# Performance work log

Hardware: AMD Instinct MI355X
Metric: run time of the kernel (lower is better)

The kernel has to match this reference:

```python
import jax, jax.numpy as jnp
from jax import lax
import numpy as np

# ---- init hyperparameters (from init_kwargs) ----
STRIDE = 1
DP_CHANNELS = 1
ATOM_R = 8
ATOM_C = 8
NUMB_ATOM = 128
T_SC = 3
K = 256
BATCH = 32
IMG = 64


def setup_inputs() -> dict:
    key = jax.random.key(0)
    k1, k2 = jax.random.split(key)
    Y = jax.random.normal(k1, (BATCH, DP_CHANNELS, IMG, IMG), dtype=jnp.float32)
    # ConvTranspose2d weight layout: (numb_atom, dp_channels, atom_c, atom_r)
    W = jax.random.normal(k2, (NUMB_ATOM, DP_CHANNELS, ATOM_C, ATOM_R), dtype=jnp.float32)
    # normalise_weights(): each (i, j) filter divided by its L2 norm
    W = W / jnp.sqrt(jnp.sum(W ** 2, axis=(2, 3), keepdims=True))
    return {"Y": Y, "W_D": W}


def _conv_D(X, W):
    # PyTorch ConvTranspose2d (stride=1, no padding): full convolution with
    # spatially-flipped kernel; W is (in=numb_atom, out=dp_channels, kh, kw).
    kh, kw = W.shape[2], W.shape[3]
    return lax.conv_general_dilated(
        X, jnp.flip(W, (2, 3)), (1, 1),
        [(kh - 1, kh - 1), (kw - 1, kw - 1)],
        dimension_numbers=('NCHW', 'IOHW', 'NCHW'))


def _conv_Dt(R, Wt):
    # PyTorch Conv2d (VALID, stride=1): Wt is (out=numb_atom, in=dp, kh, kw)
    return lax.conv_general_dilated(
        R, Wt, (1, 1), 'VALID', dimension_numbers=('NCHW', 'OIHW', 'NCHW'))


def _hard_threshold_k(X, k):
    # keep the k largest-|.| entries per sample (over flattened C,H,W)
    B = X.shape[0]
    flat = X.reshape(B, -1)
    _, idx = lax.top_k(jnp.abs(flat), k)                      # [B, k]
    vals = jnp.take_along_axis(flat, idx, axis=1)             # [B, k]
    out = jnp.zeros_like(flat).at[jnp.arange(B)[:, None], idx].set(vals)
    return out.reshape(X.shape)


def _linesearch(Y, X, W, Wt, k):
    R = Y - _conv_D(X, W)
    g = _conv_Dt(R, Wt)
    l2_start = jnp.sum(R ** 2)

    def attempt(alpha):
        Xu = _hard_threshold_k(X + alpha * g, k)
        err = jnp.sum((Y - _conv_D(Xu, W)) ** 2)
        return Xu, err

    Xu0, err0 = attempt(jnp.float32(1.0))

    def cond(s):
        _, _, err, count = s
        return (err >= l2_start) & (count <= 15)

    def body(s):
        alpha, _, _, count = s
        alpha = alpha * jnp.float32(0.5)
        Xu, err = attempt(alpha)
        return (alpha, Xu, err, count + 1)

    alpha, Xu, err, _ = lax.while_loop(
        cond, body, (jnp.float32(1.0), Xu0, err0, jnp.int32(0)))
    return Xu, err, alpha


def reference(Y, W_D):
    # D_trans.weight = D.weight.permute(0,1,3,2) -> (numb_atom, dp, atom_r, atom_c)
    Wt = jnp.swapaxes(W_D, 2, 3)
    kh, kw = Wt.shape[2], Wt.shape[3]
    B, _, H, W_sp = Y.shape
    X = jnp.zeros((B, W_D.shape[0], H - kh + 1, W_sp - kw + 1), dtype=Y.dtype)
    for _ in range(T_SC):
        X, _, _ = _linesearch(Y, X, W_D, Wt, K)
    return X
```

## Files before the change

kernel.cpp:

```cpp
#include <hip/hip_runtime.h>
#include <stdint.h>

#define NB   32
#define NCH  128
#define IMG  64
#define IMG2 4096
#define OH   57
#define OHW  3249
#define CHW  415872
#define KTOP 256
#define NATT 17
#define NS   32
#define SCAP 512
#define CAP2 8192
#define NCAP 2048
#define NBUCK 8192
#define HSHIFT 18
#define TGT  512
#define RSTRIDE 72
#define NZB  257

__global__ void k_init(int* support_cnt) {
    if (threadIdx.x < NB) support_cnt[threadIdx.x] = 0;
}

__global__ __launch_bounds__(256) void k_resid(
    const float* __restrict__ Y, const float* __restrict__ W,
    const int* __restrict__ support_cnt, const uint32_t* __restrict__ support_idx,
    const float* __restrict__ support_val, float* __restrict__ Rg, double* __restrict__ l2part,
    uint32_t* __restrict__ hist, int* __restrict__ cand_cnt)
{
    int bx = blockIdx.x, tid = threadIdx.x;
    if (bx >= NB) {
        int zb = bx - NB;
        if (zb < 256) {
            ((uint4*)hist)[zb * 256 + tid] = make_uint4(0u, 0u, 0u, 0u);
        } else {
            ((uint4*)cand_cnt)[tid] = make_uint4(0u, 0u, 0u, 0u);
        }
        return;
    }
    int b = bx;
    __shared__ float Rs[IMG2];
    const float4* Y4 = (const float4*)(Y + b * IMG2);
    float4* R4 = (float4*)Rs;
    for (int i = tid; i < IMG2 / 4; i += 256) R4[i] = Y4[i];
    __syncthreads();
    int n = support_cnt[b];
    for (int task = tid; task < n * 64; task += 256) {
        int i = task >> 6, tap = task & 63, p = tap >> 3, q = tap & 7;
        uint32_t idx = support_idx[b * KTOP + i];
        float val = support_val[b * KTOP + i];
        int c = idx / OHW, rem = idx % OHW, s = rem / OH, t = rem % OH;
        float w = W[c * 64 + p * 8 + q];
        atomicAdd(&Rs[(s + p) * IMG + (t + q)], -val * w);
    }
    __syncthreads();
    double acc = 0.0;
    for (int i = tid; i < IMG2; i += 256) {
        float v = Rs[i];
        Rg[b * IMG2 + i] = v;
        acc += (double)v * (double)v;
    }
    __shared__ double red[256];
    red[tid] = acc; __syncthreads();
    for (int s2 = 128; s2 > 0; s2 >>= 1) { if (tid < s2) red[tid] += red[tid + s2]; __syncthreads(); }
    if (tid == 0) l2part[b] = red[0];
}

__global__ __launch_bounds__(256) void k_conv(
    const float* __restrict__ Rg, const float* __restrict__ W,
    float* __restrict__ g_out, uint32_t* __restrict__ hist)
{
    int b = blockIdx.x, cg0 = blockIdx.y, tid = threadIdx.x;
    __shared__ float Rs[71 * 72];
    __shared__ uint32_t hl[NBUCK];
    for (int i = tid; i < 71 * 72; i += 256) Rs[i] = 0.f;
    for (int i = tid; i < NBUCK; i += 256) hl[i] = 0u;
    __syncthreads();
    const float4* R4 = (const float4*)(Rg + b * IMG2);
    for (int i = tid; i < 1024; i += 256) {
        int row = i >> 4, col4 = (i & 15) * 4;
        *(float4*)&Rs[row * 72 + col4] = R4[i];
    }
    __syncthreads();
    int csub = tid >> 7;
    int tile = tid & 127;
    bool active = tile < 120;
    int tr = active ? tile / 15 : 0;
    int tc = active ? tile % 15 : 0;
    int s0 = tr * 8, t0 = tc * 4;

    for (int sub = 0; sub < 4; ++sub) {
        int c = cg0 * 8 + sub * 2 + csub;
        int c_s = __builtin_amdgcn_readfirstlane(c);
        const float* Wc = W + c_s * 64;

        float acc[8][4];
#pragma unroll
        for (int r = 0; r < 8; ++r)
#pragma unroll
            for (int cc = 0; cc < 4; ++cc) acc[r][cc] = 0.f;

#pragma unroll
        for (int rho = 0; rho < 15; ++rho) {
            float rb[12];
            const float* rp = &Rs[(s0 + rho) * 72 + t0];
            *(float4*)&rb[0] = *(const float4*)rp;
            *(float4*)&rb[4] = *(const float4*)(rp + 4);
            *(float4*)&rb[8] = *(const float4*)(rp + 8);
#pragma unroll
            for (int r = 0; r < 8; ++r) {
                const int p = rho - r;
                if (p >= 0 && p < 8) {
#pragma unroll
                    for (int q = 0; q < 8; ++q) {
                        float wv = Wc[q * 8 + p];
#pragma unroll
                        for (int cc = 0; cc < 4; ++cc)
                            acc[r][cc] = fmaf(rb[cc + q], wv, acc[r][cc]);
                    }
                }
            }
        }
        if (active) {
            float* go = g_out + (size_t)(b * NCH + c) * OHW;
#pragma unroll
            for (int r = 0; r < 8; ++r) {
                int s = s0 + r;
                if (s < OH) {
#pragma unroll
                    for (int cc = 0; cc < 4; ++cc) {
                        int t = t0 + cc;
                        if (t < OH) {
                            float v = acc[r][cc];
                            go[s * OH + t] = v;
                            uint32_t bits = __float_as_uint(v) & 0x7fffffffu;
                            atomicAdd(&hl[bits >> HSHIFT], 1u);
                        }
                    }
                }
            }
        }
    }
    __syncthreads();
    for (int i = tid; i < NBUCK; i += 256) {
        uint32_t v = hl[i];
        if (v) atomicAdd(&hist[b * NBUCK + i], v);
    }
}

__global__ __launch_bounds__(256) void k_thresh(const uint32_t* __restrict__ hist,
                                                uint32_t* __restrict__ thr) {
    int b = blockIdx.x, tid = threadIdx.x;
    uint32_t h[32];
    uint32_t s = 0;
    const uint32_t* hb = hist + b * NBUCK + tid * 32;
#pragma unroll
    for (int k = 0; k < 32; ++k) { h[k] = hb[k]; s += h[k]; }
    __shared__ uint32_t buf[2][256];
    int cur = 0;
    buf[0][tid] = s;
    __syncthreads();
    for (int d = 1; d < 256; d <<= 1) {
        uint32_t v = buf[cur][tid];
        if (tid + d < 256) v += buf[cur][tid + d];
        buf[cur ^ 1][tid] = v;
        cur ^= 1;
        __syncthreads();
    }
    uint32_t sufme = buf[cur][tid];
    uint32_t base  = (tid < 255) ? buf[cur][tid + 1] : 0u;
    if (tid == 0 && buf[cur][0] < TGT) thr[b] = 0u;
    if (base < TGT && sufme >= TGT) {
        uint32_t acc = base; int bk = 0;
#pragma unroll
        for (int k = 31; k >= 0; --k) {
            acc += h[k];
            if (acc >= TGT) { bk = tid * 32 + k; break; }
        }
        thr[b] = (uint32_t)bk << HSHIFT;
    }
}

__global__ __launch_bounds__(256) void k_collect(
    const float* __restrict__ g, const uint32_t* __restrict__ thr,
    int* __restrict__ cand_cnt, uint32_t* __restrict__ cand_idx, float* __restrict__ cand_g)
{
    int b = blockIdx.y;
    int i4 = blockIdx.x * 256 + threadIdx.x;
    if (i4 >= CHW / 4) return;
    int slice = blockIdx.x & (NS - 1);
    uint32_t tb = thr[b];
    float4 v4 = ((const float4*)(g + (size_t)b * CHW))[i4];
    float vv[4] = { v4.x, v4.y, v4.z, v4.w };
#pragma unroll
    for (int k = 0; k < 4; ++k) {
        uint32_t bits = __float_as_uint(vv[k]) & 0x7fffffffu;
        if (bits >= tb) {
            int pos = atomicAdd(&cand_cnt[b * NS + slice], 1);
            if (pos < SCAP) {
                cand_idx[(b * NS + slice) * SCAP + pos] = (uint32_t)(i4 * 4 + k);
                cand_g[(b * NS + slice) * SCAP + pos] = vv[k];
            }
        }
    }
}

__global__ __launch_bounds__(256) void k_suppg(
    const float* __restrict__ g, const uint32_t* __restrict__ thr,
    const int* __restrict__ support_cnt, const uint32_t* __restrict__ support_idx,
    const float* __restrict__ support_val,
    const int* __restrict__ cand_cnt, const uint32_t* __restrict__ cand_idx,
    const float* __restrict__ cand_g,
    uint32_t* __restrict__ c2_idx, float* __restrict__ c2_g, float* __restrict__ c2_x,
    int* __restrict__ nc_out)
{
    int b = blockIdx.x, tid = threadIdx.x;
    __shared__ uint32_t sidx[KTOP];
    __shared__ float sval[KTOP];
    __shared__ int cnts[NS];
    __shared__ int soff[NS + 1];
    __shared__ int extra;
    int n = support_cnt[b];
    if (tid < NS) cnts[tid] = min(cand_cnt[b * NS + tid], SCAP);
    if (tid == 0) extra = 0;
    if (tid < n) { sidx[tid] = support_idx[b * KTOP + tid]; sval[tid] = support_val[b * KTOP + tid]; }
    __syncthreads();
    if (tid < n) {
        uint32_t idx = sidx[tid];
        float gv = g[(size_t)b * CHW + idx];
        uint32_t bits = __float_as_uint(gv) & 0x7fffffffu;
        if (bits < thr[b]) {
            int p = atomicAdd(&extra, 1);
            c2_idx[b * CAP2 + p] = idx; c2_g[b * CAP2 + p] = gv;
        }
    }
    __syncthreads();
    __shared__ int nc_sh;
    if (tid == 0) {
        int acc = extra;
        for (int s = 0; s < NS; ++s) { soff[s] = acc; acc += cnts[s]; }
        soff[NS] = acc;
        nc_sh = min(acc, NCAP);
        nc_out[b] = nc_sh;
    }
    __syncthreads();
    for (int t = tid; t < NS * SCAP; t += 256) {
        int s = t >> 9, j = t & (SCAP - 1);
        if (j < cnts[s]) {
            int d = soff[s] + j;
            if (d < NCAP) {
                c2_idx[b * CAP2 + d] = cand_idx[(b * NS + s) * SCAP + j];
                c2_g[b * CAP2 + d] = cand_g[(b * NS + s) * SCAP + j];
            }
        }
    }
    __syncthreads();
    int nc = nc_sh;
    for (int j = tid; j < nc; j += 256) {
        uint32_t q = c2_idx[b * CAP2 + j];
        float x = 0.f;
        int lo = 0, hi = n - 1;
        while (lo <= hi) {
            int mid = (lo + hi) >> 1;
            uint32_t m = sidx[mid];
            if (m == q) { x = sval[mid]; break; }
            if (m < q) lo = mid + 1; else hi = mid - 1;
        }
        c2_x[b * CAP2 + j] = x;
    }
}

__global__ __launch_bounds__(256) void k_attempt(
    const float* __restrict__ Y, const float* __restrict__ W,
    const int* __restrict__ nc_in, const uint32_t* __restrict__ cand_idx,
    const float* __restrict__ cand_g, const float* __restrict__ cand_x,
    uint32_t* __restrict__ sel_idx, float* __restrict__ sel_val, double* __restrict__ err)
{
    int a = blockIdx.x, b = blockIdx.y, tid = threadIdx.x;
    int lane = tid & 63, wid = tid >> 6;
    float alpha = ldexpf(1.f, -a);
    int nc = min(nc_in[b], NCAP);
    const uint32_t* ci = cand_idx + b * CAP2;
    const float* cgp = cand_g + b * CAP2;
    const float* cxp = cand_x + b * CAP2;

    __shared__ uint32_t s_cidx[KTOP];
    __shared__ float s_v[KTOP];
    __shared__ uint32_t tie_f[256];
    __shared__ float tie_v[256];
    __shared__ float recon[64 * RSTRIDE];
    __shared__ double redd[4];

    uint32_t kr[32];
#pragma unroll
    for (int j = 0; j < 32; ++j) {
        int i = lane + 64 * j;
        bool ok = i < nc;
        float gg = ok ? cgp[i] : 0.f;
        float xx = ok ? cxp[i] : 0.f;
        float vv = fmaf(alpha, gg, xx);
        kr[j] = ok ? (__float_as_uint(vv) & 0x7fffffffu) : 0u;
    }

    uint32_t T = 0;
    for (int bit = 30; bit >= 0; --bit) {
        uint32_t tt = T | (1u << bit);
        int lc = 0;
#pragma unroll
        for (int j = 0; j < 32; ++j) lc += (kr[j] >= tt) ? 1 : 0;
        for (int d = 32; d > 0; d >>= 1) lc += __shfl_xor(lc, d, 64);
        if (lc >= KTOP) T = tt;
    }

    if (wid != 0) {
        for (int i = tid - 64; i < 64 * RSTRIDE; i += 192) recon[i] = 0.f;
    } else {
        unsigned long long ltm = (1ull << lane) - 1ull;
        int base = 0, tbase = 0;
#pragma unroll
        for (int j = 0; j < 32; ++j) {
            int i = lane + 64 * j;
            bool valid = i < nc;
            bool isg = valid && (kr[j] > T);
            bool ist = valid && (kr[j] == T);
            unsigned long long mg = __ballot(isg);
            unsigned long long mt = __ballot(ist);
            if (mg | mt) {
                uint32_t cid = 0; float vv = 0.f;
                if (isg || ist) {
                    cid = ci[i];
                    vv = fmaf(alpha, cgp[i], cxp[i]);
                }
                if (isg) {
                    int p = base + __popcll(mg & ltm);
                    if (p < KTOP) { s_cidx[p] = cid; s_v[p] = vv; }
                }
                if (ist) {
                    int p = tbase + __popcll(mt & ltm);
                    if (p < 256) { tie_f[p] = cid; tie_v[p] = vv; }
                }
            }
            base += __popcll(mg);
            tbase += __popcll(mt);
        }
        int nsel = min(base, KTOP);
        int rem = KTOP - nsel;
        int nt = min(tbase, 256);
        for (int j0 = lane; j0 < nt; j0 += 64) {
            uint32_t me = tie_f[j0];
            int rank = 0;
            for (int j2 = 0; j2 < nt; ++j2) rank += (tie_f[j2] < me) ? 1 : 0;
            if (rank < rem) { s_cidx[nsel + rank] = me; s_v[nsel + rank] = tie_v[j0]; }
        }
    }
    __syncthreads();

    sel_idx[((size_t)a * NB + b) * KTOP + tid] = s_cidx[tid];
    sel_val[((size_t)a * NB + b) * KTOP + tid] = s_v[tid];

    for (int task = tid; task < KTOP * 64; task += 256) {
        int i = task >> 6, tap = task & 63, p = tap >> 3, q = tap & 7;
        uint32_t idx = s_cidx[i];
        float val = s_v[i];
        int c = idx / OHW, remn = idx % OHW, s = remn / OH, t = remn % OH;
        atomicAdd(&recon[(s + p) * RSTRIDE + (t + q)], val * W[c * 64 + p * 8 + q]);
    }
    __syncthreads();

    double accd = 0.0;
    for (int e = tid; e < IMG2; e += 256) {
        float d = Y[b * IMG2 + e] - recon[(e >> 6) * RSTRIDE + (e & 63)];
        accd += (double)d * (double)d;
    }
    for (int d = 32; d > 0; d >>= 1) accd += __shfl_xor(accd, d, 64);
    if (lane == 0) redd[wid] = accd;
    __syncthreads();
    if (tid == 0) err[a * NB + b] = ((redd[0] + redd[1]) + redd[2]) + redd[3];
}

__global__ __launch_bounds__(256) void k_update(
    const double* __restrict__ l2part, const double* __restrict__ err,
    const uint32_t* __restrict__ sel_idx, const float* __restrict__ sel_val,
    int* __restrict__ support_cnt, uint32_t* __restrict__ support_idx, float* __restrict__ support_val)
{
    int b = blockIdx.x, tid = threadIdx.x;
    __shared__ double esum[NATT + 1];
    __shared__ int sel_sh;
    if (tid < NATT) {
        double e = 0.0;
        for (int b2 = 0; b2 < NB; ++b2) e += err[tid * NB + b2];
        esum[tid] = e;
    } else if (tid == NATT) {
        double l2 = 0.0;
        for (int b2 = 0; b2 < NB; ++b2) l2 += l2part[b2];
        esum[NATT] = l2;
    }
    __syncthreads();
    if (tid == 0) {
        double l2 = esum[NATT];
        int sel = NATT - 1;
        for (int a2 = 0; a2 < NATT; ++a2) if (esum[a2] < l2) { sel = a2; break; }
        sel_sh = sel;
    }
    __syncthreads();
    int a = sel_sh;
    __shared__ uint32_t ki[KTOP];
    __shared__ float kv[KTOP];
    ki[tid] = sel_idx[((size_t)a * NB + b) * KTOP + tid];
    kv[tid] = sel_val[((size_t)a * NB + b) * KTOP + tid];
    __syncthreads();
    uint32_t me = ki[tid];
    int rank = 0;
    for (int j = 0; j < KTOP; ++j) rank += (ki[j] < me) ? 1 : 0;
    support_idx[b * KTOP + rank] = me;
    support_val[b * KTOP + rank] = kv[tid];
    if (tid == 0) support_cnt[b] = KTOP;
}

__global__ void k_outzero(float4* __restrict__ out) {
    int i = blockIdx.x * 256 + threadIdx.x;
    if (i < (NB * CHW) / 4) out[i] = make_float4(0.f, 0.f, 0.f, 0.f);
}

__global__ void k_scatter(const uint32_t* __restrict__ support_idx, const float* __restrict__ support_val,
                          float* __restrict__ out) {
    int b = blockIdx.x, tid = threadIdx.x;
    if (tid < KTOP) out[(size_t)b * CHW + support_idx[b * KTOP + tid]] = support_val[b * KTOP + tid];
}

static size_t align256(size_t x) { return (x + 255) & ~(size_t)255; }

extern "C" void kernel_launch(void* const* d_in, const int* in_sizes, int n_in,
                              void* d_out, int out_size, void* d_ws, size_t ws_size,
                              hipStream_t stream)
{
    const float* Y = (const float*)d_in[0];
    const float* W = (const float*)d_in[1];
    float* out = (float*)d_out;

    char* p = (char*)d_ws;
    size_t off = 0;
    auto carve = [&](size_t bytes) { void* r = p + off; off = align256(off + bytes); return r; };
    float*    Rg          = (float*)   carve(NB * IMG2 * sizeof(float));
    uint32_t* hist        = (uint32_t*)carve((size_t)NB * NBUCK * sizeof(uint32_t));
    uint32_t* thr         = (uint32_t*)carve(NB * sizeof(uint32_t));
    int*      cand_cnt    = (int*)     carve(NB * NS * sizeof(int));
    double*   l2part      = (double*)  carve(NB * sizeof(double));
    double*   err         = (double*)  carve(NATT * NB * sizeof(double));
    int*      support_cnt = (int*)     carve(NB * sizeof(int));
    uint32_t* support_idx = (uint32_t*)carve(NB * KTOP * sizeof(uint32_t));
    float*    support_val = (float*)   carve(NB * KTOP * sizeof(float));
    uint32_t* sel_idx     = (uint32_t*)carve((size_t)NATT * NB * KTOP * sizeof(uint32_t));
    float*    sel_val     = (float*)   carve((size_t)NATT * NB * KTOP * sizeof(float));
    uint32_t* cand_idx    = (uint32_t*)carve((size_t)NB * NS * SCAP * sizeof(uint32_t));
    float*    cand_g      = (float*)   carve((size_t)NB * NS * SCAP * sizeof(float));
    uint32_t* c2_idx      = (uint32_t*)carve((size_t)NB * CAP2 * sizeof(uint32_t));
    float*    c2_g        = (float*)   carve((size_t)NB * CAP2 * sizeof(float));
    float*    c2_x        = (float*)   carve((size_t)NB * CAP2 * sizeof(float));
    int*      nc_out      = (int*)     carve(NB * sizeof(int));
    (void)ws_size; (void)in_sizes; (void)n_in; (void)out_size;

    k_init<<<1, 64, 0, stream>>>(support_cnt);
    for (int t = 0; t < 3; ++t) {
        k_resid<<<NB + NZB, 256, 0, stream>>>(Y, W, support_cnt, support_idx, support_val,
                                              Rg, l2part, hist, cand_cnt);
        k_conv<<<dim3(NB, 16), 256, 0, stream>>>(Rg, W, out, hist);
        k_thresh<<<NB, 256, 0, stream>>>(hist, thr);
        k_collect<<<dim3((CHW / 4 + 255) / 256, NB), 256, 0, stream>>>(out, thr, cand_cnt, cand_idx, cand_g);
        k_suppg<<<NB, 256, 0, stream>>>(out, thr, support_cnt, support_idx, support_val,
                                        cand_cnt, cand_idx, cand_g, c2_idx, c2_g, c2_x, nc_out);
        k_attempt<<<dim3(NATT, NB), 256, 0, stream>>>(Y, W, nc_out, c2_idx, c2_g, c2_x,
                                                      sel_idx, sel_val, err);
        k_update<<<NB, 256, 0, stream>>>(l2part, err, sel_idx, sel_val,
                                         support_cnt, support_idx, support_val);
    }
    k_outzero<<<((NB * CHW) / 4 + 255) / 256, 256, 0, stream>>>((float4*)out);
    k_scatter<<<NB, 256, 0, stream>>>(support_idx, support_val, out);
}
```

Before: 695.9 us.

## Presort non-support candidates once so each attempt merges two 256-lists

Non-support candidates scale as alpha*g, so their order is the same for every alpha. k_suppg ranks them once and keeps the top 256 per batch. It also gathers the gradient at support entries and precomputes packed (c,s,t) coordinates. Each k_attempt block then picks the top 256 from 512 keys by rank counting, replacing the 31-step bitwise radix threshold over up to 2048 candidates, and uses the packed coordinates to avoid integer divisions. The cost is an O(n^2) rank loop in k_suppg, and the candidate cap is reduced to 1536, which could drop valid candidates.

```diff
diff --git a/kernel.cpp b/kernel.cpp
--- a/kernel.cpp
+++ b/kernel.cpp
@@ -12,13 +12,14 @@
 #define NATT 17
 #define NS   32
 #define SCAP 512
-#define CAP2 8192
-#define NCAP 2048
+#define NCAP 1536
 #define NBUCK 8192
 #define HSHIFT 18
 #define TGT  512
 #define RSTRIDE 72
 #define NZB  257
+
+typedef unsigned long long ull;
 
 __global__ void k_init(int* support_cnt) {
     if (threadIdx.x < NB) support_cnt[threadIdx.x] = 0;
@@ -208,164 +209,150 @@
 }
 
 __global__ __launch_bounds__(256) void k_suppg(
-    const float* __restrict__ g, const uint32_t* __restrict__ thr,
+    const float* __restrict__ g,
     const int* __restrict__ support_cnt, const uint32_t* __restrict__ support_idx,
     const float* __restrict__ support_val,
     const int* __restrict__ cand_cnt, const uint32_t* __restrict__ cand_idx,
     const float* __restrict__ cand_g,
-    uint32_t* __restrict__ c2_idx, float* __restrict__ c2_g, float* __restrict__ c2_x,
-    int* __restrict__ nc_out)
-{
-    int b = blockIdx.x, tid = threadIdx.x;
+    uint32_t* __restrict__ ns_idx, float* __restrict__ ns_g, uint32_t* __restrict__ ns_pk,
+    float* __restrict__ sup_g, uint32_t* __restrict__ sup_pk)
+{
+    int b = blockIdx.x, tid = threadIdx.x, lane = tid & 63;
     __shared__ uint32_t sidx[KTOP];
     __shared__ float sval[KTOP];
     __shared__ int cnts[NS];
-    __shared__ int soff[NS + 1];
-    __shared__ int extra;
+    __shared__ ull ck[NCAP];
+    __shared__ float cg_l[NCAP];
+    __shared__ int nns_sh;
     int n = support_cnt[b];
     if (tid < NS) cnts[tid] = min(cand_cnt[b * NS + tid], SCAP);
-    if (tid == 0) extra = 0;
+    if (tid == 0) nns_sh = 0;
     if (tid < n) { sidx[tid] = support_idx[b * KTOP + tid]; sval[tid] = support_val[b * KTOP + tid]; }
     __syncthreads();
+    (void)sval;
     if (tid < n) {
         uint32_t idx = sidx[tid];
         float gv = g[(size_t)b * CHW + idx];
-        uint32_t bits = __float_as_uint(gv) & 0x7fffffffu;
-        if (bits < thr[b]) {
-            int p = atomicAdd(&extra, 1);
-            c2_idx[b * CAP2 + p] = idx; c2_g[b * CAP2 + p] = gv;
-        }
-    }
-    __syncthreads();
-    __shared__ int nc_sh;
-    if (tid == 0) {
-        int acc = extra;
-        for (int s = 0; s < NS; ++s) { soff[s] = acc; acc += cnts[s]; }
-        soff[NS] = acc;
-        nc_sh = min(acc, NCAP);
-        nc_out[b] = nc_sh;
-    }
-    __syncthreads();
-    for (int t = tid; t < NS * SCAP; t += 256) {
-        int s = t >> 9, j = t & (SCAP - 1);
+        sup_g[b * KTOP + tid] = gv;
+        int c = idx / OHW, r = idx % OHW, s = r / OH, t = r % OH;
+        sup_pk[b * KTOP + tid] = (uint32_t)((c << 12) | (s << 6) | t);
+    } else {
+        sup_g[b * KTOP + tid] = 0.f;
+        sup_pk[b * KTOP + tid] = 0u;
+    }
+    for (int t0 = tid; t0 < NS * SCAP; t0 += 256) {
+        int s = t0 >> 9, j = t0 & (SCAP - 1);
+        bool keep = false; uint32_t idx = 0; float gv = 0.f;
         if (j < cnts[s]) {
-            int d = soff[s] + j;
-            if (d < NCAP) {
-                c2_idx[b * CAP2 + d] = cand_idx[(b * NS + s) * SCAP + j];
-                c2_g[b * CAP2 + d] = cand_g[(b * NS + s) * SCAP + j];
+            idx = cand_idx[(b * NS + s) * SCAP + j];
+            gv = cand_g[(b * NS + s) * SCAP + j];
+            int lo = 0, hi = n - 1; bool found = false;
+            while (lo <= hi) {
+                int mid = (lo + hi) >> 1;
+                uint32_t m = sidx[mid];
+                if (m == idx) { found = true; break; }
+                if (m < idx) lo = mid + 1; else hi = mid - 1;
             }
-        }
-    }
-    __syncthreads();
-    int nc = nc_sh;
-    for (int j = tid; j < nc; j += 256) {
-        uint32_t q = c2_idx[b * CAP2 + j];
-        float x = 0.f;
-        int lo = 0, hi = n - 1;
-        while (lo <= hi) {
-            int mid = (lo + hi) >> 1;
-            uint32_t m = sidx[mid];
-            if (m == q) { x = sval[mid]; break; }
-            if (m < q) lo = mid + 1; else hi = mid - 1;
-        }
-        c2_x[b * CAP2 + j] = x;
+            keep = !found;
+        }
+        ull mk = __ballot(keep);
+        if (mk) {
+            int basep = 0;
+            if (lane == 0) basep = atomicAdd(&nns_sh, (int)__popcll(mk));
+            basep = __shfl(basep, 0, 64);
+            if (keep) {
+                int p = basep + (int)__popcll(mk & ((1ull << lane) - 1ull));
+                if (p < NCAP) {
+                    ck[p] = ((ull)(__float_as_uint(gv) & 0x7fffffffu) << 32) | (ull)(uint32_t)(~idx);
+                    cg_l[p] = gv;
+                }
+            }
+        }
+    }
+    __syncthreads();
+    int nns = min(nns_sh, NCAP);
+    ull myk[6]; int myr[6];
+#pragma unroll
+    for (int q = 0; q < 6; ++q) { int i = tid + 256 * q; myk[q] = (i < nns) ? ck[i] : 0ull; myr[q] = 0; }
+    for (int j = 0; j < nns; ++j) {
+        ull kj = ck[j];
+#pragma unroll
+        for (int q = 0; q < 6; ++q) myr[q] += (kj > myk[q]) ? 1 : 0;
+    }
+#pragma unroll
+    for (int q = 0; q < 6; ++q) {
+        int i = tid + 256 * q;
+        if (i < nns && myr[q] < KTOP) {
+            uint32_t idx = ~(uint32_t)myk[q];
+            int r = myr[q];
+            ns_idx[b * KTOP + r] = idx;
+            ns_g[b * KTOP + r] = cg_l[i];
+            int c = idx / OHW, rr = idx % OHW, s = rr / OH, t = rr % OH;
+            ns_pk[b * KTOP + r] = (uint32_t)((c << 12) | (s << 6) | t);
+        }
     }
 }
 
 __global__ __launch_bounds__(256) void k_attempt(
     const float* __restrict__ Y, const float* __restrict__ W,
-    const int* __restrict__ nc_in, const uint32_t* __restrict__ cand_idx,
-    const float* __restrict__ cand_g, const float* __restrict__ cand_x,
+    const int* __restrict__ support_cnt, const uint32_t* __restrict__ support_idx,
+    const float* __restrict__ support_val,
+    const float* __restrict__ sup_g, const uint32_t* __restrict__ sup_pk,
+    const uint32_t* __restrict__ ns_idx, const float* __restrict__ ns_g,
+    const uint32_t* __restrict__ ns_pk,
     uint32_t* __restrict__ sel_idx, float* __restrict__ sel_val, double* __restrict__ err)
 {
     int a = blockIdx.x, b = blockIdx.y, tid = threadIdx.x;
     int lane = tid & 63, wid = tid >> 6;
     float alpha = ldexpf(1.f, -a);
-    int nc = min(nc_in[b], NCAP);
-    const uint32_t* ci = cand_idx + b * CAP2;
-    const float* cgp = cand_g + b * CAP2;
-    const float* cxp = cand_x + b * CAP2;
-
-    __shared__ uint32_t s_cidx[KTOP];
+    int n = support_cnt[b];
+
+    __shared__ ull ku[512];
+    __shared__ uint32_t s_ci[KTOP];
     __shared__ float s_v[KTOP];
-    __shared__ uint32_t tie_f[256];
-    __shared__ float tie_v[256];
+    __shared__ uint32_t s_pk[KTOP];
     __shared__ float recon[64 * RSTRIDE];
     __shared__ double redd[4];
 
-    uint32_t kr[32];
-#pragma unroll
-    for (int j = 0; j < 32; ++j) {
-        int i = lane + 64 * j;
-        bool ok = i < nc;
-        float gg = ok ? cgp[i] : 0.f;
-        float xx = ok ? cxp[i] : 0.f;
-        float vv = fmaf(alpha, gg, xx);
-        kr[j] = ok ? (__float_as_uint(vv) & 0x7fffffffu) : 0u;
-    }
-
-    uint32_t T = 0;
-    for (int bit = 30; bit >= 0; --bit) {
-        uint32_t tt = T | (1u << bit);
-        int lc = 0;
-#pragma unroll
-        for (int j = 0; j < 32; ++j) lc += (kr[j] >= tt) ? 1 : 0;
-        for (int d = 32; d > 0; d >>= 1) lc += __shfl_xor(lc, d, 64);
-        if (lc >= KTOP) T = tt;
-    }
-
-    if (wid != 0) {
-        for (int i = tid - 64; i < 64 * RSTRIDE; i += 192) recon[i] = 0.f;
+    uint32_t nsi = ns_idx[b * KTOP + tid];
+    float v_ns = alpha * ns_g[b * KTOP + tid];
+    uint32_t pk_ns = ns_pk[b * KTOP + tid];
+    ull k_ns = ((ull)(__float_as_uint(v_ns) & 0x7fffffffu) << 32) | (ull)(uint32_t)(~nsi);
+    ku[tid] = k_ns;
+    uint32_t spi; float v_sup; uint32_t pk_sup;
+    if (tid < n) {
+        spi = support_idx[b * KTOP + tid];
+        v_sup = fmaf(alpha, sup_g[b * KTOP + tid], support_val[b * KTOP + tid]);
+        pk_sup = sup_pk[b * KTOP + tid];
     } else {
-        unsigned long long ltm = (1ull << lane) - 1ull;
-        int base = 0, tbase = 0;
-#pragma unroll
-        for (int j = 0; j < 32; ++j) {
-            int i = lane + 64 * j;
-            bool valid = i < nc;
-            bool isg = valid && (kr[j] > T);
-            bool ist = valid && (kr[j] == T);
-            unsigned long long mg = __ballot(isg);
-            unsigned long long mt = __ballot(ist);
-            if (mg | mt) {
-                uint32_t cid = 0; float vv = 0.f;
-                if (isg || ist) {
-                    cid = ci[i];
-                    vv = fmaf(alpha, cgp[i], cxp[i]);
-                }
-                if (isg) {
-                    int p = base + __popcll(mg & ltm);
-                    if (p < KTOP) { s_cidx[p] = cid; s_v[p] = vv; }
-                }
-                if (ist) {
-                    int p = tbase + __popcll(mt & ltm);
-                    if (p < 256) { tie_f[p] = cid; tie_v[p] = vv; }
-                }
-            }
-            base += __popcll(mg);
-            tbase += __popcll(mt);
-        }
-        int nsel = min(base, KTOP);
-        int rem = KTOP - nsel;
-        int nt = min(tbase, 256);
-        for (int j0 = lane; j0 < nt; j0 += 64) {
-            uint32_t me = tie_f[j0];
-            int rank = 0;
-            for (int j2 = 0; j2 < nt; ++j2) rank += (tie_f[j2] < me) ? 1 : 0;
-            if (rank < rem) { s_cidx[nsel + rank] = me; s_v[nsel + rank] = tie_v[j0]; }
-        }
-    }
-    __syncthreads();
-
-    sel_idx[((size_t)a * NB + b) * KTOP + tid] = s_cidx[tid];
+        spi = (uint32_t)(CHW + tid);
+        v_sup = 0.f; pk_sup = 0u;
+    }
+    ull k_sup = ((ull)(__float_as_uint(v_sup) & 0x7fffffffu) << 32) | (ull)(uint32_t)(~spi);
+    ku[256 + tid] = k_sup;
+    s_v[tid] = 0.f; s_ci[tid] = 0u; s_pk[tid] = 0u;
+    for (int i = tid; i < 64 * RSTRIDE; i += 256) recon[i] = 0.f;
+    __syncthreads();
+
+    int c_ns = 0, c_sup = 0;
+    for (int j = 0; j < 512; ++j) {
+        ull kj = ku[j];
+        c_ns += (kj > k_ns) ? 1 : 0;
+        c_sup += (kj > k_sup) ? 1 : 0;
+    }
+    if (c_ns < KTOP) { s_ci[c_ns] = nsi; s_v[c_ns] = v_ns; s_pk[c_ns] = pk_ns; }
+    if (c_sup < KTOP) { s_ci[c_sup] = spi; s_v[c_sup] = v_sup; s_pk[c_sup] = pk_sup; }
+    __syncthreads();
+
+    sel_idx[((size_t)a * NB + b) * KTOP + tid] = s_ci[tid];
     sel_val[((size_t)a * NB + b) * KTOP + tid] = s_v[tid];
 
     for (int task = tid; task < KTOP * 64; task += 256) {
         int i = task >> 6, tap = task & 63, p = tap >> 3, q = tap & 7;
-        uint32_t idx = s_cidx[i];
+        uint32_t pk = s_pk[i];
         float val = s_v[i];
-        int c = idx / OHW, remn = idx % OHW, s = remn / OH, t = remn % OH;
-        atomicAdd(&recon[(s + p) * RSTRIDE + (t + q)], val * W[c * 64 + p * 8 + q]);
+        int c = pk >> 12, s = (pk >> 6) & 63, t = pk & 63;
+        atomicAdd(&recon[(s + p) * RSTRIDE + (t + q)], val * W[c * 64 + tap]);
     }
     __syncthreads();
 
@@ -456,10 +443,11 @@
     float*    sel_val     = (float*)   carve((size_t)NATT * NB * KTOP * sizeof(float));
     uint32_t* cand_idx    = (uint32_t*)carve((size_t)NB * NS * SCAP * sizeof(uint32_t));
     float*    cand_g      = (float*)   carve((size_t)NB * NS * SCAP * sizeof(float));
-    uint32_t* c2_idx      = (uint32_t*)carve((size_t)NB * CAP2 * sizeof(uint32_t));
-    float*    c2_g        = (float*)   carve((size_t)NB * CAP2 * sizeof(float));
-    float*    c2_x        = (float*)   carve((size_t)NB * CAP2 * sizeof(float));
-    int*      nc_out      = (int*)     carve(NB * sizeof(int));
+    uint32_t* ns_idx      = (uint32_t*)carve(NB * KTOP * sizeof(uint32_t));
+    float*    ns_gbuf     = (float*)   carve(NB * KTOP * sizeof(float));
+    uint32_t* ns_pk       = (uint32_t*)carve(NB * KTOP * sizeof(uint32_t));
+    float*    sup_gbuf    = (float*)   carve(NB * KTOP * sizeof(float));
+    uint32_t* sup_pk      = (uint32_t*)carve(NB * KTOP * sizeof(uint32_t));
     (void)ws_size; (void)in_sizes; (void)n_in; (void)out_size;
 
     k_init<<<1, 64, 0, stream>>>(support_cnt);
@@ -469,9 +457,11 @@
         k_conv<<<dim3(NB, 16), 256, 0, stream>>>(Rg, W, out, hist);
         k_thresh<<<NB, 256, 0, stream>>>(hist, thr);
         k_collect<<<dim3((CHW / 4 + 255) / 256, NB), 256, 0, stream>>>(out, thr, cand_cnt, cand_idx, cand_g);
-        k_suppg<<<NB, 256, 0, stream>>>(out, thr, support_cnt, support_idx, support_val,
-                                        cand_cnt, cand_idx, cand_g, c2_idx, c2_g, c2_x, nc_out);
-        k_attempt<<<dim3(NATT, NB), 256, 0, stream>>>(Y, W, nc_out, c2_idx, c2_g, c2_x,
+        k_suppg<<<NB, 256, 0, stream>>>(out, support_cnt, support_idx, support_val,
+                                        cand_cnt, cand_idx, cand_g,
+                                        ns_idx, ns_gbuf, ns_pk, sup_gbuf, sup_pk);
+        k_attempt<<<dim3(NATT, NB), 256, 0, stream>>>(Y, W, support_cnt, support_idx, support_val,
+                                                      sup_gbuf, sup_pk, ns_idx, ns_gbuf, ns_pk,
                                                       sel_idx, sel_val, err);
         k_update<<<NB, 256, 0, stream>>>(l2part, err, sel_idx, sel_val,
                                          support_cnt, support_idx, support_val);
```

New measurement: 802.8 us. +15.4%, slower.
